# Kernel tuning notes

Measured on AMD Instinct MI355X. Metric: run time of the kernel, lower is better.

## Reference

```python
import jax, jax.numpy as jnp
import numpy as np

# PGA G(3,0,1) blade layout: [1, e0,e1,e2,e3, e01,e02,e03,e12,e13,e23, e012,e013,e023,e123, e0123]
GRADE_IDX = np.array([0,1,1,1,1,2,2,2,2,2,2,3,3,3,3,4])  # grade of each of the 16 blades
INNER_IDX = np.array([0,2,3,4,8,9,10,14])  # non-degenerate blades (no e0) used by invariant inner product
POINT_IDX = np.array([11,12,13])           # trivector point coordinates e012,e013,e023
EPS = 1e-6

def equi_linear(x, W5, b):
    # x: [B,N,Cin,16]; W5: [5,Cout,Cin] grade-wise channel mixing (equivariant)
    Wc = W5[GRADE_IDX]                       # [16,Cout,Cin]
    y = jnp.einsum('bnic,coi->bnoc', x, Wc)  # [B,N,Cout,16]
    return y.at[..., 0].add(b)               # bias only on scalar blade

def equi_rms_norm(x, w):
    # RMS of per-channel multivector norms, averaged over channels
    ms = jnp.mean(jnp.sum(x * x, axis=-1), axis=-1, keepdims=True)  # [B,N,1]
    return x * jax.lax.rsqrt(ms + EPS)[..., None] * w[:, None]

def setup_inputs():
    key = jax.random.key(0)
    ks = jax.random.split(key, 10)
    B, Nq, Nk, C, H = 8, 1024, 256, 48, 8
    s = 0.05
    return {
        'hidden': jax.random.normal(ks[0], (B, Nq, C, 16), jnp.float32),
        'vision_embedding': jax.random.normal(ks[1], (B, Nk, C, 16), jnp.float32),
        'ln_w': jnp.ones((C,), jnp.float32),
        'Wq': jax.random.normal(ks[2], (5, H * C, C), jnp.float32) * s,
        'bq': jnp.zeros((H * C,), jnp.float32),
        'Wkv': jax.random.normal(ks[3], (5, 2 * H * C, C), jnp.float32) * s,
        'bkv': jnp.zeros((2 * H * C,), jnp.float32),
        'Wo': jax.random.normal(ks[4], (5, C, H * C), jnp.float32) * s,
        'bo': jnp.zeros((C,), jnp.float32),
        'daa_scale': jnp.zeros((H,), jnp.float32),
    }

def reference(hidden, vision_embedding, ln_w, Wq, bq, Wkv, bkv, Wo, bo, daa_scale):
    B, Nq, C, _ = hidden.shape
    H = daa_scale.shape[0]
    normed = equi_rms_norm(hidden, ln_w)
    q = equi_linear(normed, Wq, bq).reshape(B, Nq, H, C, 16)
    kv = equi_linear(vision_embedding, Wkv, bkv)
    Nk = kv.shape[1]
    kv = kv.reshape(B, Nk, 2, H, C, 16)
    k, v = kv[:, :, 0], kv[:, :, 1]
    # inner-product attention (ipa) over non-degenerate blades
    qi, ki = q[..., INNER_IDX], k[..., INNER_IDX]
    ipa = jnp.einsum('bqhcj,bkhcj->bhqk', qi, ki) / np.sqrt(8.0 * C)
    # distance-aware attention (daa) on trivector point coords, expanded ||q-k||^2
    qp, kp = q[..., POINT_IDX], k[..., POINT_IDX]
    q2 = jnp.sum(qp * qp, axis=(-1, -2)).transpose(0, 2, 1)  # [B,H,Nq]
    k2 = jnp.sum(kp * kp, axis=(-1, -2)).transpose(0, 2, 1)  # [B,H,Nk]
    cross = jnp.einsum('bqhcj,bkhcj->bhqk', qp, kp)
    dist2 = q2[..., :, None] + k2[..., None, :] - 2.0 * cross
    daa = -jax.nn.softplus(daa_scale)[None, :, None, None] * dist2 / C
    attn = jax.nn.softmax(ipa + daa, axis=-1)                 # [B,H,Nq,Nk]
    out = jnp.einsum('bhqk,bkhcj->bqhcj', attn, v).reshape(B, Nq, H * C, 16)
    return hidden + equi_linear(out, Wo, bo)
```

## Files before the change

### kernel.cpp

```cpp
#include <hip/hip_runtime.h>

typedef unsigned short u16;
typedef unsigned int u32;
typedef unsigned long long u64;

typedef float f32x4 __attribute__((ext_vector_type(4)));
typedef short bf16x8 __attribute__((ext_vector_type(8)));

#define BB 8
#define NQ 1024
#define NK 256
#define HH 8
#define KD 544

__device__ __forceinline__ float bf2f(u16 u) {
  union { u32 i; float f; } v; v.i = ((u32)u) << 16; return v.f;
}
__device__ __forceinline__ u16 f2bf(float f) {
  union { u32 i; float f; } v; v.f = f;
  u32 i = v.i;
  return (u16)((i + 0x7FFFu + ((i >> 16) & 1u)) >> 16);
}
__device__ __forceinline__ float softplusf(float d) {
  return (d > 20.f) ? d : log1pf(__expf(d));
}

#define GRADE_TAB 0x4333322222211110ULL
#define ACT_TAB   0xDCBEA984320ULL
__device__ __forceinline__ int grade_of(int c) { return (int)((GRADE_TAB >> (c * 4)) & 15ULL); }
__device__ __forceinline__ int act_of(int s) { return (int)((ACT_TAB >> (s * 4)) & 15ULL); }

constexpr float INV_S384 = 0.05103103630798288f;

__global__ __launch_bounds__(256) void wB_kernel(
    const float* __restrict__ Wq, const float* __restrict__ Wkv,
    const float* __restrict__ Wo, u16* __restrict__ WqB,
    u16* __restrict__ WkvB, u16* __restrict__ WoB) {
  int idx = blockIdx.x * 256 + threadIdx.x;
  const int NA = 5 * 384 * 64, NB = 5 * 768 * 64, NC = 5 * 48 * 384;
  if (idx < NA) {
    int g = idx / (384 * 64);
    int rem = idx - g * 384 * 64;
    int o = rem >> 6, j = rem & 63;
    WqB[idx] = (j < 48) ? f2bf(Wq[((size_t)g * 384 + o) * 48 + j]) : (u16)0;
  } else if (idx < NA + NB) {
    int k = idx - NA;
    int g = k / (768 * 64);
    int rem = k - g * 768 * 64;
    int o = rem >> 6, j = rem & 63;
    WkvB[k] = (j < 48) ? f2bf(Wkv[((size_t)g * 768 + o) * 48 + j]) : (u16)0;
  } else if (idx < NA + NB + NC) {
    int k = idx - NA - NB;
    WoB[k] = f2bf(Wo[k]);
  }
}

__global__ __launch_bounds__(256) void xJ_kernel(
    const float* __restrict__ src, u16* __restrict__ dst,
    const float* __restrict__ lnw, int NR, int norm) {
  __shared__ __align__(16) float ls[16 * 772];
  __shared__ float rs_s[16];
  const int t = threadIdx.x;
  const int row0 = blockIdx.x * 64;
  const int row16 = t & 15, c = t >> 4;
  for (int chunk = 0; chunk < 4; chunk++) {
    const int r0c = row0 + chunk * 16;
    __syncthreads();
#pragma unroll
    for (int k = 0; k < 12; k++) {
      int f = t + 256 * k;
      int r = f / 192, j = f - r * 192;
      *(float4*)&ls[r * 772 + j * 4] =
          *(const float4*)(src + (size_t)(r0c + r) * 768 + j * 4);
    }
    __syncthreads();
    if (norm) {
      const int r = t >> 4, j16 = t & 15;
      float s = 0.f;
#pragma unroll
      for (int i = 0; i < 12; i++) {
        float4 v = *(const float4*)&ls[r * 772 + j16 * 48 + i * 4];
        s += v.x * v.x + v.y * v.y + v.z * v.z + v.w * v.w;
      }
#pragma unroll
      for (int off = 8; off; off >>= 1) s += __shfl_xor(s, off, 16);
      if (j16 == 0) rs_s[r] = rsqrtf(s * (1.f / 48.f) + 1e-6f);
      __syncthreads();
    }
    const float rsv = norm ? rs_s[row16] : 1.f;
    u16 buf[64];
#pragma unroll
    for (int i = 0; i < 48; i++) {
      float v = ls[row16 * 772 + i * 16 + c];
      if (norm) v *= rsv * lnw[i];
      buf[i] = f2bf(v);
    }
#pragma unroll
    for (int i = 48; i < 64; i++) buf[i] = 0;
    u16* dp = dst + ((size_t)c * NR + r0c + row16) * 64;
#pragma unroll
    for (int j4 = 0; j4 < 8; j4++) *(uint4*)(dp + j4 * 8) = *(uint4*)&buf[j4 * 8];
  }
}

#define QSTR 392
__global__ __launch_bounds__(256) void q_mfma(
    const u16* __restrict__ xq, const u16* __restrict__ WqB,
    const float* __restrict__ bq, const float* __restrict__ daa,
    u16* __restrict__ qsel) {
  __shared__ __align__(16) u16 es[4 * 16 * QSTR];
  const int t = threadIdx.x;
  const int w = t >> 6, lane = t & 63, m16 = lane & 15, quad = lane >> 4;
  const int slot = blockIdx.y;
  const int c = act_of(slot), g = grade_of(c);
  const int row0 = blockIdx.x * 64;
  const int b = row0 >> 10, n0 = row0 & 1023;
  f32x4 acc[24];
#pragma unroll
  for (int nt = 0; nt < 24; nt++) acc[nt] = (f32x4)0.f;
  const u16* ap = xq + ((size_t)c * 8192 + row0 + w * 16 + m16) * 64 + quad * 8;
  const u16* wb = WqB + (size_t)g * 384 * 64 + (size_t)m16 * 64 + quad * 8;
#pragma unroll
  for (int ks = 0; ks < 2; ks++) {
    bf16x8 af = *(const bf16x8*)(ap + ks * 32);
#pragma unroll
    for (int nt = 0; nt < 24; nt++) {
      bf16x8 bf = *(const bf16x8*)(wb + (size_t)nt * 16 * 64 + ks * 32);
      acc[nt] = __builtin_amdgcn_mfma_f32_16x16x32_bf16(af, bf, acc[nt], 0, 0, 0);
    }
  }
#pragma unroll
  for (int nt = 0; nt < 24; nt++) {
    const int o = nt * 16 + m16;
    const int h = o / 48;
    const float sc = (slot < 8) ? INV_S384 : (2.f * softplusf(daa[h]) * (1.f / 48.f));
    const float bias = (slot == 0) ? bq[o] : 0.f;
#pragma unroll
    for (int rr = 0; rr < 4; rr++)
      es[(w * 16 + quad * 4 + rr) * QSTR + o] = f2bf((acc[nt][rr] + bias) * sc);
  }
  __syncthreads();
  for (int ch = t; ch < 512; ch += 256) {
    int r = ch >> 3, h = ch & 7;
    const uint4* sr = (const uint4*)&es[r * QSTR + h * 48];
    u16* dst = qsel + ((size_t)(b * 8 + h) * NQ + n0 + r) * KD + slot * 48;
#pragma unroll
    for (int j = 0; j < 6; j++) ((uint4*)dst)[j] = sr[j];
    if (slot == 10) {
      uint4 z = {0u, 0u, 0u, 0u};
      ((uint4*)dst)[6] = z;
      ((uint4*)dst)[7] = z;
    }
  }
}

#define VSTR 72
__global__ __launch_bounds__(256) void kv_mfma(
    const u16* __restrict__ xv, const u16* __restrict__ WkvB,
    const float* __restrict__ bkv, u16* __restrict__ ksel,
    u16* __restrict__ vT) {
  __shared__ __align__(16) u16 es[384 * VSTR];
  const int t = threadIdx.x;
  const int w = t >> 6, lane = t & 63, m16 = lane & 15, quad = lane >> 4;
  const int task = blockIdx.y;
  const int row0 = blockIdx.x * 64;
  const int b = row0 >> 8, n0 = row0 & 255;

  if (task < 11) {
    const int c = act_of(task), g = grade_of(c);
    f32x4 acc[24];
#pragma unroll
    for (int nt = 0; nt < 24; nt++) acc[nt] = (f32x4)0.f;
    const u16* ap = xv + ((size_t)c * 2048 + row0 + w * 16 + m16) * 64 + quad * 8;
    const u16* wb = WkvB + (size_t)g * 768 * 64 + (size_t)m16 * 64 + quad * 8;
#pragma unroll
    for (int ks = 0; ks < 2; ks++) {
      bf16x8 af = *(const bf16x8*)(ap + ks * 32);
#pragma unroll
      for (int nt = 0; nt < 24; nt++) {
        bf16x8 bf = *(const bf16x8*)(wb + (size_t)nt * 16 * 64 + ks * 32);
        acc[nt] = __builtin_amdgcn_mfma_f32_16x16x32_bf16(af, bf, acc[nt], 0, 0, 0);
      }
    }
#pragma unroll
    for (int nt = 0; nt < 24; nt++) {
      const int o = nt * 16 + m16;
      const float bias = (task == 0) ? bkv[o] : 0.f;
#pragma unroll
      for (int rr = 0; rr < 4; rr++)
        es[(w * 16 + quad * 4 + rr) * QSTR + o] = f2bf(acc[nt][rr] + bias);
    }
    __syncthreads();
    for (int ch = t; ch < 512; ch += 256) {
      int r = ch >> 3, h = ch & 7;
      const uint4* sr = (const uint4*)&es[r * QSTR + h * 48];
      u16* dst = ksel + ((size_t)(b * 8 + h) * NK + n0 + r) * KD + task * 48;
#pragma unroll
      for (int j = 0; j < 6; j++) ((uint4*)dst)[j] = sr[j];
      if (task == 10) {
        uint4 z = {0u, 0u, 0u, 0u};
        ((uint4*)dst)[6] = z;
        ((uint4*)dst)[7] = z;
      }
    }
  } else {
    const int c = task - 11, g = grade_of(c);
    f32x4 acc[24];
#pragma unroll
    for (int nt = 0; nt < 24; nt++) acc[nt] = (f32x4)0.f;
    const u16* ap = xv + ((size_t)c * 2048 + row0 + w * 16 + m16) * 64 + quad * 8;
    const u16* wb = WkvB + (size_t)g * 768 * 64 + (size_t)(384 + m16) * 64 + quad * 8;
#pragma unroll
    for (int ks = 0; ks < 2; ks++) {
      bf16x8 af = *(const bf16x8*)(ap + ks * 32);
#pragma unroll
      for (int nt = 0; nt < 24; nt++) {
        bf16x8 bf = *(const bf16x8*)(wb + (size_t)nt * 16 * 64 + ks * 32);
        acc[nt] = __builtin_amdgcn_mfma_f32_16x16x32_bf16(af, bf, acc[nt], 0, 0, 0);
      }
    }
#pragma unroll
    for (int nt = 0; nt < 24; nt++) {
      const int o = nt * 16 + m16;
      const float bias = (c == 0) ? bkv[384 + o] : 0.f;
#pragma unroll
      for (int rr = 0; rr < 4; rr++)
        es[o * VSTR + w * 16 + quad * 4 + rr] = f2bf(acc[nt][rr] + bias);
    }
    __syncthreads();
    for (int id = t; id < 6144; id += 256) {
      int o = id >> 4, part = id & 15;
      uint2 v = *(const uint2*)&es[o * VSTR + part * 4];
      int h = o / 48, oc = o - h * 48;
      *(uint2*)(vT + ((size_t)(b * 8 + h) * 768 + oc * 16 + c) * 256 + n0 + part * 4) = v;
    }
  }
}

__global__ __launch_bounds__(256) void k2_kernel(const u16* __restrict__ ksel,
                                                 const float* __restrict__ daa,
                                                 float* __restrict__ kbias) {
  int id = blockIdx.x * 256 + threadIdx.x;
  const uint4* p = (const uint4*)(ksel + (size_t)id * KD + 384);
  float s = 0.f;
#pragma unroll
  for (int j = 0; j < 18; j++) {
    uint4 v = p[j];
    u32 a[4] = {v.x, v.y, v.z, v.w};
#pragma unroll
    for (int q = 0; q < 4; q++) {
      float lo = bf2f((u16)(a[q] & 0xFFFFu));
      float hi = bf2f((u16)(a[q] >> 16));
      s += lo * lo + hi * hi;
    }
  }
  int h = (id >> 8) & 7;
  kbias[id] = -(softplusf(daa[h]) * (1.f / 48.f)) * s;
}

#define SPBW 268
#define STGW 26

#define QK_MFMA_BLOCK(AQ0, AQ1, AQ2, AQ3, AK0, AK1, AK2, AK3)                 \
  sacc[0][0] = __builtin_amdgcn_mfma_f32_16x16x32_bf16(AQ0, AK0, sacc[0][0], 0, 0, 0); \
  sacc[1][0] = __builtin_amdgcn_mfma_f32_16x16x32_bf16(AQ1, AK0, sacc[1][0], 0, 0, 0); \
  sacc[2][0] = __builtin_amdgcn_mfma_f32_16x16x32_bf16(AQ2, AK0, sacc[2][0], 0, 0, 0); \
  sacc[3][0] = __builtin_amdgcn_mfma_f32_16x16x32_bf16(AQ3, AK0, sacc[3][0], 0, 0, 0); \
  sacc[0][1] = __builtin_amdgcn_mfma_f32_16x16x32_bf16(AQ0, AK1, sacc[0][1], 0, 0, 0); \
  sacc[1][1] = __builtin_amdgcn_mfma_f32_16x16x32_bf16(AQ1, AK1, sacc[1][1], 0, 0, 0); \
  sacc[2][1] = __builtin_amdgcn_mfma_f32_16x16x32_bf16(AQ2, AK1, sacc[2][1], 0, 0, 0); \
  sacc[3][1] = __builtin_amdgcn_mfma_f32_16x16x32_bf16(AQ3, AK1, sacc[3][1], 0, 0, 0); \
  sacc[0][2] = __builtin_amdgcn_mfma_f32_16x16x32_bf16(AQ0, AK2, sacc[0][2], 0, 0, 0); \
  sacc[1][2] = __builtin_amdgcn_mfma_f32_16x16x32_bf16(AQ1, AK2, sacc[1][2], 0, 0, 0); \
  sacc[2][2] = __builtin_amdgcn_mfma_f32_16x16x32_bf16(AQ2, AK2, sacc[2][2], 0, 0, 0); \
  sacc[3][2] = __builtin_amdgcn_mfma_f32_16x16x32_bf16(AQ3, AK2, sacc[3][2], 0, 0, 0); \
  sacc[0][3] = __builtin_amdgcn_mfma_f32_16x16x32_bf16(AQ0, AK3, sacc[0][3], 0, 0, 0); \
  sacc[1][3] = __builtin_amdgcn_mfma_f32_16x16x32_bf16(AQ1, AK3, sacc[1][3], 0, 0, 0); \
  sacc[2][3] = __builtin_amdgcn_mfma_f32_16x16x32_bf16(AQ2, AK3, sacc[2][3], 0, 0, 0); \
  sacc[3][3] = __builtin_amdgcn_mfma_f32_16x16x32_bf16(AQ3, AK3, sacc[3][3], 0, 0, 0);

__global__ __launch_bounds__(256, 2) void attn_kernel(
    const u16* __restrict__ qsel, const u16* __restrict__ ksel,
    const float* __restrict__ kbias, const u16* __restrict__ vT,
    u16* __restrict__ ctxJ) {
  const int qt = blockIdx.x, h = blockIdx.y, b = blockIdx.z;
  const int g = b * 8 + h;

  const int t = threadIdx.x;
  const int w = t >> 6;
  const int lane = t & 63;
  const int m16 = lane & 15;
  const int quad = lane >> 4;

  __shared__ __align__(16) u32 uni_s[13312];
  u16* spb = (u16*)uni_s;
  u32* stg = uni_s;
  __shared__ float kb[256];
  __shared__ __align__(16) float wred[64][4];
  __shared__ __align__(16) float wsum[64][4];

  const size_t bh = (size_t)g;
  const int n0 = qt * 64;
  const u16* qg = qsel + (bh * NQ + n0) * KD;
  const u16* kg = ksel + bh * NK * KD;
  const u16* vg = vT + bh * 768 * 256;

  kb[t] = kbias[bh * NK + t];
  __syncthreads();
  float kbr[4];
#pragma unroll
  for (int nt = 0; nt < 4; nt++) kbr[nt] = kb[w * 64 + nt * 16 + m16];

  f32x4 sacc[4][4];
#pragma unroll
  for (int mt = 0; mt < 4; mt++)
#pragma unroll
    for (int nt = 0; nt < 4; nt++) sacc[mt][nt] = (f32x4)0.f;

  const u16* qp0 = qg + (size_t)m16 * KD + quad * 8;
  const u16* qp1 = qg + (size_t)(16 + m16) * KD + quad * 8;
  const u16* qp2 = qg + (size_t)(32 + m16) * KD + quad * 8;
  const u16* qp3 = qg + (size_t)(48 + m16) * KD + quad * 8;
  const u16* kp = kg + (size_t)(w * 64 + m16) * KD + quad * 8;
  bf16x8 cq0 = *(const bf16x8*)qp0;
  bf16x8 cq1 = *(const bf16x8*)qp1;
  bf16x8 cq2 = *(const bf16x8*)qp2;
  bf16x8 cq3 = *(const bf16x8*)qp3;
  bf16x8 ck0 = *(const bf16x8*)(kp);
  bf16x8 ck1 = *(const bf16x8*)(kp + 16 * KD);
  bf16x8 ck2 = *(const bf16x8*)(kp + 32 * KD);
  bf16x8 ck3 = *(const bf16x8*)(kp + 48 * KD);
  bf16x8 dq0 = *(const bf16x8*)(qp0 + 32);
  bf16x8 dq1 = *(const bf16x8*)(qp1 + 32);
  bf16x8 dq2 = *(const bf16x8*)(qp2 + 32);
  bf16x8 dq3 = *(const bf16x8*)(qp3 + 32);
  bf16x8 dk0 = *(const bf16x8*)(kp + 32);
  bf16x8 dk1 = *(const bf16x8*)(kp + 16 * KD + 32);
  bf16x8 dk2 = *(const bf16x8*)(kp + 32 * KD + 32);
  bf16x8 dk3 = *(const bf16x8*)(kp + 48 * KD + 32);
  for (int i = 0; i < 7; i++) {
    const int oA = (2 * i + 2) * 32;
    bf16x8 nq0 = *(const bf16x8*)(qp0 + oA);
    bf16x8 nq1 = *(const bf16x8*)(qp1 + oA);
    bf16x8 nq2 = *(const bf16x8*)(qp2 + oA);
    bf16x8 nq3 = *(const bf16x8*)(qp3 + oA);
    bf16x8 nk0 = *(const bf16x8*)(kp + oA);
    bf16x8 nk1 = *(const bf16x8*)(kp + 16 * KD + oA);
    bf16x8 nk2 = *(const bf16x8*)(kp + 32 * KD + oA);
    bf16x8 nk3 = *(const bf16x8*)(kp + 48 * KD + oA);
    const int oB = (2 * i + 3) * 32;
    bf16x8 mq0 = *(const bf16x8*)(qp0 + oB);
    bf16x8 mq1 = *(const bf16x8*)(qp1 + oB);
    bf16x8 mq2 = *(const bf16x8*)(qp2 + oB);
    bf16x8 mq3 = *(const bf16x8*)(qp3 + oB);
    bf16x8 mk0 = *(const bf16x8*)(kp + oB);
    bf16x8 mk1 = *(const bf16x8*)(kp + 16 * KD + oB);
    bf16x8 mk2 = *(const bf16x8*)(kp + 32 * KD + oB);
    bf16x8 mk3 = *(const bf16x8*)(kp + 48 * KD + oB);
    QK_MFMA_BLOCK(cq0, cq1, cq2, cq3, ck0, ck1, ck2, ck3)
    QK_MFMA_BLOCK(dq0, dq1, dq2, dq3, dk0, dk1, dk2, dk3)
    cq0 = nq0; cq1 = nq1; cq2 = nq2; cq3 = nq3;
    ck0 = nk0; ck1 = nk1; ck2 = nk2; ck3 = nk3;
    dq0 = mq0; dq1 = mq1; dq2 = mq2; dq3 = mq3;
    dk0 = mk0; dk1 = mk1; dk2 = mk2; dk3 = mk3;
  }
  {
    const int oT = 16 * 32;
    bf16x8 nq0 = *(const bf16x8*)(qp0 + oT);
    bf16x8 nq1 = *(const bf16x8*)(qp1 + oT);
    bf16x8 nq2 = *(const bf16x8*)(qp2 + oT);
    bf16x8 nq3 = *(const bf16x8*)(qp3 + oT);
    bf16x8 nk0 = *(const bf16x8*)(kp + oT);
    bf16x8 nk1 = *(const bf16x8*)(kp + 16 * KD + oT);
    bf16x8 nk2 = *(const bf16x8*)(kp + 32 * KD + oT);
    bf16x8 nk3 = *(const bf16x8*)(kp + 48 * KD + oT);
    QK_MFMA_BLOCK(cq0, cq1, cq2, cq3, ck0, ck1, ck2, ck3)
    QK_MFMA_BLOCK(dq0, dq1, dq2, dq3, dk0, dk1, dk2, dk3)
    QK_MFMA_BLOCK(nq0, nq1, nq2, nq3, nk0, nk1, nk2, nk3)
  }

#pragma unroll
  for (int mt = 0; mt < 4; mt++)
#pragma unroll
    for (int rr = 0; rr < 4; rr++) {
      float a0 = sacc[mt][0][rr] + kbr[0];
      float a1 = sacc[mt][1][rr] + kbr[1];
      float a2 = sacc[mt][2][rr] + kbr[2];
      float a3 = sacc[mt][3][rr] + kbr[3];
      sacc[mt][0][rr] = a0; sacc[mt][1][rr] = a1;
      sacc[mt][2][rr] = a2; sacc[mt][3][rr] = a3;
      float m = fmaxf(fmaxf(a0, a1), fmaxf(a2, a3));
#pragma unroll
      for (int off = 1; off < 16; off <<= 1)
        m = fmaxf(m, __shfl_xor(m, off));
      if (m16 == mt * 4 + rr) wred[mt * 16 + quad * 4 + rr][w] = m;
    }
  __syncthreads();
#pragma unroll
  for (int mt = 0; mt < 4; mt++)
#pragma unroll
    for (int rr = 0; rr < 4; rr++) {
      const int row = mt * 16 + quad * 4 + rr;
      float4 m4 = *(const float4*)wred[row];
      const float gm = fmaxf(fmaxf(m4.x, m4.y), fmaxf(m4.z, m4.w));
      float s = 0.f;
#pragma unroll
      for (int nt = 0; nt < 4; nt++) {
        float e = __expf(sacc[mt][nt][rr] - gm);
        s += e;
        spb[row * SPBW + w * 64 + nt * 16 + m16] = f2bf(e);
      }
#pragma unroll
      for (int off = 1; off < 16; off <<= 1)
        s += __shfl_xor(s, off);
      if (m16 == mt * 4 + rr) wsum[row][w] = s;
    }
  __syncthreads();

  f32x4 oacc[4][12];
#pragma unroll
  for (int mt = 0; mt < 4; mt++)
#pragma unroll
    for (int nt = 0; nt < 12; nt++) oacc[mt][nt] = (f32x4)0.f;

  const u16* vp = vg + (size_t)(w * 192 + m16) * 256 + quad * 8;
  bf16x8 vc[12];
#pragma unroll
  for (int nt = 0; nt < 12; nt++)
    vc[nt] = *(const bf16x8*)(vp + (size_t)nt * 16 * 256);
#pragma unroll
  for (int ks = 0; ks < 8; ks++) {
    bf16x8 vn[12];
    if (ks < 7) {
#pragma unroll
      for (int nt = 0; nt < 12; nt++)
        vn[nt] = *(const bf16x8*)(vp + (size_t)nt * 16 * 256 + (ks + 1) * 32);
    }
    bf16x8 pa0 = *(const bf16x8*)(&spb[(size_t)m16 * SPBW + ks * 32 + quad * 8]);
    bf16x8 pa1 = *(const bf16x8*)(&spb[(size_t)(16 + m16) * SPBW + ks * 32 + quad * 8]);
    bf16x8 pa2 = *(const bf16x8*)(&spb[(size_t)(32 + m16) * SPBW + ks * 32 + quad * 8]);
    bf16x8 pa3 = *(const bf16x8*)(&spb[(size_t)(48 + m16) * SPBW + ks * 32 + quad * 8]);
#pragma unroll
    for (int nt = 0; nt < 12; nt++) {
      oacc[0][nt] = __builtin_amdgcn_mfma_f32_16x16x32_bf16(pa0, vc[nt], oacc[0][nt], 0, 0, 0);
      oacc[1][nt] = __builtin_amdgcn_mfma_f32_16x16x32_bf16(pa1, vc[nt], oacc[1][nt], 0, 0, 0);
      oacc[2][nt] = __builtin_amdgcn_mfma_f32_16x16x32_bf16(pa2, vc[nt], oacc[2][nt], 0, 0, 0);
      oacc[3][nt] = __builtin_amdgcn_mfma_f32_16x16x32_bf16(pa3, vc[nt], oacc[3][nt], 0, 0, 0);
    }
    if (ks < 7) {
#pragma unroll
      for (int nt = 0; nt < 12; nt++) vc[nt] = vn[nt];
    }
  }

  const size_t rowbase = (size_t)b * NQ + n0;
#pragma unroll
  for (int ch2 = 0; ch2 < 2; ch2++) {
    __syncthreads();
    if ((m16 >> 3) == ch2) {
      const int c8 = m16 & 7;
#pragma unroll
      for (int mt = 0; mt < 4; mt++)
#pragma unroll
        for (int rr = 0; rr < 4; rr++) {
          const int row = mt * 16 + quad * 4 + rr;
          float4 s4 = *(const float4*)wsum[row];
          const float iv = 1.f / (s4.x + s4.y + s4.z + s4.w);
          u32* dp = stg + (row * 8 + c8) * STGW + w * 6;
#pragma unroll
          for (int j = 0; j < 6; j++) {
            u32 lo = f2bf(oacc[mt][2 * j][rr] * iv);
            u32 hi = f2bf(oacc[mt][2 * j + 1][rr] * iv);
            dp[j] = lo | (hi << 16);
          }
        }
    }
    __syncthreads();
    for (int ch = t; ch < 512; ch += 256) {
      const int prow = ch >> 3, pc8 = ch & 7;
      const u32* sp2 = stg + (prow * 8 + pc8) * STGW;
      u16* dst = ctxJ + ((size_t)(ch2 * 8 + pc8) * 8192 + rowbase + prow) * 384 + h * 48;
#pragma unroll
      for (int j6 = 0; j6 < 6; j6++) {
        uint2 a = *(const uint2*)(sp2 + j6 * 4);
        uint2 bb2 = *(const uint2*)(sp2 + j6 * 4 + 2);
        uint4 v4v = {a.x, a.y, bb2.x, bb2.y};
        *(uint4*)(dst + j6 * 8) = v4v;
      }
    }
  }
}

#define ESTR2 785
__global__ __launch_bounds__(1024) void out_kernel(
    const u16* __restrict__ ctxJ, const u16* __restrict__ WoB,
    const float* __restrict__ bo, const float* __restrict__ hidden,
    float* __restrict__ out) {
  __shared__ __align__(16) float es[16 * ESTR2];
  const int t = threadIdx.x;
  const int c = __builtin_amdgcn_readfirstlane(t >> 6);
  const int lane = t & 63;
  const int m16 = lane & 15, quad = lane >> 4;
  const int r0 = blockIdx.x * 16;
  const int g = grade_of(c);
  const u16* wb = WoB + (size_t)g * 48 * 384;

  f32x4 acc[3];
#pragma unroll
  for (int nt = 0; nt < 3; nt++) acc[nt] = (f32x4)0.f;
  const u16* ap = ctxJ + ((size_t)c * 8192 + r0 + m16) * 384 + quad * 8;
#pragma unroll 4
  for (int ks = 0; ks < 12; ks++) {
    bf16x8 af = *(const bf16x8*)(ap + ks * 32);
#pragma unroll
    for (int nt = 0; nt < 3; nt++) {
      bf16x8 bf = *(const bf16x8*)(wb + (size_t)(nt * 16 + m16) * 384 + ks * 32 + quad * 8);
      acc[nt] = __builtin_amdgcn_mfma_f32_16x16x32_bf16(af, bf, acc[nt], 0, 0, 0);
    }
  }
  __syncthreads();
#pragma unroll
  for (int nt = 0; nt < 3; nt++)
#pragma unroll
    for (int rr = 0; rr < 4; rr++)
      es[(quad * 4 + rr) * ESTR2 + c * 49 + nt * 16 + m16] = acc[nt][rr];
  __syncthreads();
#pragma unroll
  for (int k = 0; k < 3; k++) {
    int m4 = t + 1024 * k;
    int r = m4 / 192;
    int col0 = (m4 - r * 192) * 4;
    int o = col0 >> 4, cb = col0 & 15;
    const float* er = &es[r * ESTR2 + o];
    float4 v;
    v.x = er[(cb + 0) * 49];
    v.y = er[(cb + 1) * 49];
    v.z = er[(cb + 2) * 49];
    v.w = er[(cb + 3) * 49];
    if (cb == 0) v.x += bo[o];
    size_t gidx = (size_t)(r0 + r) * 768 + col0;
    const float4 hv = *(const float4*)&hidden[gidx];
    v.x += hv.x; v.y += hv.y; v.z += hv.z; v.w += hv.w;
    *(float4*)&out[gidx] = v;
  }
}

extern "C" void kernel_launch(void* const* d_in, const int* in_sizes, int n_in,
                              void* d_out, int out_size, void* d_ws, size_t ws_size,
                              hipStream_t stream) {
  const float* hidden = (const float*)d_in[0];
  const float* vis = (const float*)d_in[1];
  const float* lnw = (const float*)d_in[2];
  const float* Wq = (const float*)d_in[3];
  const float* bq = (const float*)d_in[4];
  const float* Wkv = (const float*)d_in[5];
  const float* bkv = (const float*)d_in[6];
  const float* Wo = (const float*)d_in[7];
  const float* bo = (const float*)d_in[8];
  const float* daa = (const float*)d_in[9];
  float* out = (float*)d_out;

  char* ws = (char*)d_ws;
  size_t off = 0;
  auto carve = [&](size_t bytes) -> void* {
    void* p = ws + off;
    off += (bytes + 255) & ~(size_t)255;
    return p;
  };
  u16* WqB = (u16*)carve((size_t)5 * 384 * 64 * 2);
  u16* WkvB = (u16*)carve((size_t)5 * 768 * 64 * 2);
  u16* WoB = (u16*)carve((size_t)5 * 48 * 384 * 2);
  u16* qsel = (u16*)carve((size_t)BB * HH * NQ * KD * 2);
  u16* ksel = (u16*)carve((size_t)BB * HH * NK * KD * 2);
  u16* vT = (u16*)carve((size_t)BB * HH * 768 * 256 * 2);
  float* kbias = (float*)carve((size_t)BB * HH * NK * 4);
  char* uni = (char*)carve((size_t)16 * 384 * 8192 * 2);
  u16* ctxJ = (u16*)uni;
  u16* xq = (u16*)uni;
  u16* xv = (u16*)(uni + (size_t)16 * 8192 * 64 * 2);

  wB_kernel<<<1800, 256, 0, stream>>>(Wq, Wkv, Wo, WqB, WkvB, WoB);
  xJ_kernel<<<BB * NQ / 64, 256, 0, stream>>>(hidden, xq, lnw, BB * NQ, 1);
  xJ_kernel<<<BB * NK / 64, 256, 0, stream>>>(vis, xv, nullptr, BB * NK, 0);
  kv_mfma<<<dim3(BB * NK / 64, 27), 256, 0, stream>>>(xv, WkvB, bkv, ksel, vT);
  k2_kernel<<<64, 256, 0, stream>>>(ksel, daa, kbias);
  q_mfma<<<dim3(BB * NQ / 64, 11), 256, 0, stream>>>(xq, WqB, bq, daa, qsel);
  attn_kernel<<<dim3(NQ / 64, HH, BB), 256, 0, stream>>>(qsel, ksel, kbias, vT, ctxJ);
  out_kernel<<<512, 1024, 0, stream>>>(ctxJ, WoB, bo, hidden, out);
}
```

Baseline: 443.5 us.

## Merge projection kernels and fold key-norm computation into KV projection

```diff
diff --git a/kernel.cpp b/kernel.cpp
--- a/kernel.cpp
+++ b/kernel.cpp
@@ -35,9 +35,11 @@
 __global__ __launch_bounds__(256) void wB_kernel(
     const float* __restrict__ Wq, const float* __restrict__ Wkv,
     const float* __restrict__ Wo, u16* __restrict__ WqB,
-    u16* __restrict__ WkvB, u16* __restrict__ WoB) {
+    u16* __restrict__ WkvB, u16* __restrict__ WoB,
+    float* __restrict__ kbias) {
   int idx = blockIdx.x * 256 + threadIdx.x;
   const int NA = 5 * 384 * 64, NB = 5 * 768 * 64, NC = 5 * 48 * 384;
+  if (idx < BB * HH * NK) kbias[idx] = 0.f;
   if (idx < NA) {
     int g = idx / (384 * 64);
     int rem = idx - g * 384 * 64;
@@ -56,12 +58,18 @@
 }
 
 __global__ __launch_bounds__(256) void xJ_kernel(
-    const float* __restrict__ src, u16* __restrict__ dst,
-    const float* __restrict__ lnw, int NR, int norm) {
+    const float* __restrict__ hidden, const float* __restrict__ vis,
+    u16* __restrict__ xq, u16* __restrict__ xv,
+    const float* __restrict__ lnw) {
   __shared__ __align__(16) float ls[16 * 772];
   __shared__ float rs_s[16];
   const int t = threadIdx.x;
-  const int row0 = blockIdx.x * 64;
+  const int bid = blockIdx.x;
+  const float* src;
+  u16* dst;
+  int NR, norm, row0;
+  if (bid < 128) { src = hidden; dst = xq; NR = 8192; norm = 1; row0 = bid * 64; }
+  else           { src = vis;    dst = xv; NR = 2048; norm = 0; row0 = (bid - 128) * 64; }
   const int row16 = t & 15, c = t >> 4;
   for (int chunk = 0; chunk < 4; chunk++) {
     const int r0c = row0 + chunk * 16;
@@ -104,66 +112,67 @@
 }
 
 #define QSTR 392
-__global__ __launch_bounds__(256) void q_mfma(
-    const u16* __restrict__ xq, const u16* __restrict__ WqB,
-    const float* __restrict__ bq, const float* __restrict__ daa,
-    u16* __restrict__ qsel) {
-  __shared__ __align__(16) u16 es[4 * 16 * QSTR];
-  const int t = threadIdx.x;
-  const int w = t >> 6, lane = t & 63, m16 = lane & 15, quad = lane >> 4;
-  const int slot = blockIdx.y;
-  const int c = act_of(slot), g = grade_of(c);
-  const int row0 = blockIdx.x * 64;
-  const int b = row0 >> 10, n0 = row0 & 1023;
-  f32x4 acc[24];
-#pragma unroll
-  for (int nt = 0; nt < 24; nt++) acc[nt] = (f32x4)0.f;
-  const u16* ap = xq + ((size_t)c * 8192 + row0 + w * 16 + m16) * 64 + quad * 8;
-  const u16* wb = WqB + (size_t)g * 384 * 64 + (size_t)m16 * 64 + quad * 8;
-#pragma unroll
-  for (int ks = 0; ks < 2; ks++) {
-    bf16x8 af = *(const bf16x8*)(ap + ks * 32);
-#pragma unroll
-    for (int nt = 0; nt < 24; nt++) {
-      bf16x8 bf = *(const bf16x8*)(wb + (size_t)nt * 16 * 64 + ks * 32);
-      acc[nt] = __builtin_amdgcn_mfma_f32_16x16x32_bf16(af, bf, acc[nt], 0, 0, 0);
-    }
-  }
-#pragma unroll
-  for (int nt = 0; nt < 24; nt++) {
-    const int o = nt * 16 + m16;
-    const int h = o / 48;
-    const float sc = (slot < 8) ? INV_S384 : (2.f * softplusf(daa[h]) * (1.f / 48.f));
-    const float bias = (slot == 0) ? bq[o] : 0.f;
-#pragma unroll
-    for (int rr = 0; rr < 4; rr++)
-      es[(w * 16 + quad * 4 + rr) * QSTR + o] = f2bf((acc[nt][rr] + bias) * sc);
-  }
-  __syncthreads();
-  for (int ch = t; ch < 512; ch += 256) {
-    int r = ch >> 3, h = ch & 7;
-    const uint4* sr = (const uint4*)&es[r * QSTR + h * 48];
-    u16* dst = qsel + ((size_t)(b * 8 + h) * NQ + n0 + r) * KD + slot * 48;
-#pragma unroll
-    for (int j = 0; j < 6; j++) ((uint4*)dst)[j] = sr[j];
-    if (slot == 10) {
-      uint4 z = {0u, 0u, 0u, 0u};
-      ((uint4*)dst)[6] = z;
-      ((uint4*)dst)[7] = z;
-    }
-  }
-}
-
 #define VSTR 72
-__global__ __launch_bounds__(256) void kv_mfma(
-    const u16* __restrict__ xv, const u16* __restrict__ WkvB,
-    const float* __restrict__ bkv, u16* __restrict__ ksel,
-    u16* __restrict__ vT) {
+__global__ __launch_bounds__(256) void qkv_mfma(
+    const u16* __restrict__ xq, const u16* __restrict__ xv,
+    const u16* __restrict__ WqB, const u16* __restrict__ WkvB,
+    const float* __restrict__ bq, const float* __restrict__ bkv,
+    const float* __restrict__ daa, u16* __restrict__ qsel,
+    u16* __restrict__ ksel, u16* __restrict__ vT,
+    float* __restrict__ kbias) {
   __shared__ __align__(16) u16 es[384 * VSTR];
   const int t = threadIdx.x;
   const int w = t >> 6, lane = t & 63, m16 = lane & 15, quad = lane >> 4;
-  const int task = blockIdx.y;
-  const int row0 = blockIdx.x * 64;
+  const int bid = blockIdx.x;
+
+  if (bid < 1408) {
+    const int rowblk = bid & 127, slot = bid >> 7;
+    const int c = act_of(slot), g = grade_of(c);
+    const int row0 = rowblk * 64;
+    const int b = row0 >> 10, n0 = row0 & 1023;
+    f32x4 acc[24];
+#pragma unroll
+    for (int nt = 0; nt < 24; nt++) acc[nt] = (f32x4)0.f;
+    const u16* ap = xq + ((size_t)c * 8192 + row0 + w * 16 + m16) * 64 + quad * 8;
+    const u16* wb = WqB + (size_t)g * 384 * 64 + (size_t)m16 * 64 + quad * 8;
+#pragma unroll
+    for (int ks = 0; ks < 2; ks++) {
+      bf16x8 af = *(const bf16x8*)(ap + ks * 32);
+#pragma unroll
+      for (int nt = 0; nt < 24; nt++) {
+        bf16x8 bf = *(const bf16x8*)(wb + (size_t)nt * 16 * 64 + ks * 32);
+        acc[nt] = __builtin_amdgcn_mfma_f32_16x16x32_bf16(af, bf, acc[nt], 0, 0, 0);
+      }
+    }
+#pragma unroll
+    for (int nt = 0; nt < 24; nt++) {
+      const int o = nt * 16 + m16;
+      const int h = o / 48;
+      const float sc = (slot < 8) ? INV_S384 : (2.f * softplusf(daa[h]) * (1.f / 48.f));
+      const float bias = (slot == 0) ? bq[o] : 0.f;
+#pragma unroll
+      for (int rr = 0; rr < 4; rr++)
+        es[(w * 16 + quad * 4 + rr) * QSTR + o] = f2bf((acc[nt][rr] + bias) * sc);
+    }
+    __syncthreads();
+    for (int ch = t; ch < 512; ch += 256) {
+      int r = ch >> 3, h = ch & 7;
+      const uint4* sr = (const uint4*)&es[r * QSTR + h * 48];
+      u16* dst = qsel + ((size_t)(b * 8 + h) * NQ + n0 + r) * KD + slot * 48;
+#pragma unroll
+      for (int j = 0; j < 6; j++) ((uint4*)dst)[j] = sr[j];
+      if (slot == 10) {
+        uint4 z = {0u, 0u, 0u, 0u};
+        ((uint4*)dst)[6] = z;
+        ((uint4*)dst)[7] = z;
+      }
+    }
+    return;
+  }
+
+  const int kvid = bid - 1408;
+  const int keyblk = kvid & 31, task = kvid >> 5;
+  const int row0 = keyblk * 64;
   const int b = row0 >> 8, n0 = row0 & 255;
 
   if (task < 11) {
@@ -203,6 +212,16 @@
         ((uint4*)dst)[7] = z;
       }
     }
+    if (task >= 8) {
+      for (int id = t; id < 512; id += 256) {
+        int r = id >> 3, hh = id & 7;
+        const u16* er = &es[r * QSTR + hh * 48];
+        float s = 0.f;
+#pragma unroll
+        for (int oc = 0; oc < 48; oc++) { float v = bf2f(er[oc]); s += v * v; }
+        atomicAdd(&kbias[((size_t)(b * 8 + hh)) * NK + n0 + r], s);
+      }
+    }
   } else {
     const int c = task - 11, g = grade_of(c);
     f32x4 acc[24];
@@ -235,27 +254,6 @@
       *(uint2*)(vT + ((size_t)(b * 8 + h) * 768 + oc * 16 + c) * 256 + n0 + part * 4) = v;
     }
   }
-}
-
-__global__ __launch_bounds__(256) void k2_kernel(const u16* __restrict__ ksel,
-                                                 const float* __restrict__ daa,
-                                                 float* __restrict__ kbias) {
-  int id = blockIdx.x * 256 + threadIdx.x;
-  const uint4* p = (const uint4*)(ksel + (size_t)id * KD + 384);
-  float s = 0.f;
-#pragma unroll
-  for (int j = 0; j < 18; j++) {
-    uint4 v = p[j];
-    u32 a[4] = {v.x, v.y, v.z, v.w};
-#pragma unroll
-    for (int q = 0; q < 4; q++) {
-      float lo = bf2f((u16)(a[q] & 0xFFFFu));
-      float hi = bf2f((u16)(a[q] >> 16));
-      s += lo * lo + hi * hi;
-    }
-  }
-  int h = (id >> 8) & 7;
-  kbias[id] = -(softplusf(daa[h]) * (1.f / 48.f)) * s;
 }
 
 #define SPBW 268
@@ -281,8 +279,8 @@
 
 __global__ __launch_bounds__(256, 2) void attn_kernel(
     const u16* __restrict__ qsel, const u16* __restrict__ ksel,
-    const float* __restrict__ kbias, const u16* __restrict__ vT,
-    u16* __restrict__ ctxJ) {
+    const float* __restrict__ kbias, const float* __restrict__ daa,
+    const u16* __restrict__ vT, u16* __restrict__ ctxJ) {
   const int qt = blockIdx.x, h = blockIdx.y, b = blockIdx.z;
   const int g = b * 8 + h;
 
@@ -305,7 +303,8 @@
   const u16* kg = ksel + bh * NK * KD;
   const u16* vg = vT + bh * 768 * 256;
 
-  kb[t] = kbias[bh * NK + t];
+  const float ksc = -(softplusf(daa[h]) * (1.f / 48.f));
+  kb[t] = ksc * kbias[bh * NK + t];
   __syncthreads();
   float kbr[4];
 #pragma unroll
@@ -579,12 +578,11 @@
   u16* xq = (u16*)uni;
   u16* xv = (u16*)(uni + (size_t)16 * 8192 * 64 * 2);
 
-  wB_kernel<<<1800, 256, 0, stream>>>(Wq, Wkv, Wo, WqB, WkvB, WoB);
-  xJ_kernel<<<BB * NQ / 64, 256, 0, stream>>>(hidden, xq, lnw, BB * NQ, 1);
-  xJ_kernel<<<BB * NK / 64, 256, 0, stream>>>(vis, xv, nullptr, BB * NK, 0);
-  kv_mfma<<<dim3(BB * NK / 64, 27), 256, 0, stream>>>(xv, WkvB, bkv, ksel, vT);
-  k2_kernel<<<64, 256, 0, stream>>>(ksel, daa, kbias);
-  q_mfma<<<dim3(BB * NQ / 64, 11), 256, 0, stream>>>(xq, WqB, bq, daa, qsel);
-  attn_kernel<<<dim3(NQ / 64, HH, BB), 256, 0, stream>>>(qsel, ksel, kbias, vT, ctxJ);
+  wB_kernel<<<1800, 256, 0, stream>>>(Wq, Wkv, Wo, WqB, WkvB, WoB, kbias);
+  xJ_kernel<<<160, 256, 0, stream>>>(hidden, vis, xq, xv, lnw);
+  qkv_mfma<<<2272, 256, 0, stream>>>(xq, xv, WqB, WkvB, bq, bkv, daa,
+                                     qsel, ksel, vT, kbias);
+  attn_kernel<<<dim3(NQ / 64, HH, BB), 256, 0, stream>>>(qsel, ksel, kbias,
+                                                          daa, vT, ctxJ);
   out_kernel<<<512, 1024, 0, stream>>>(ctxJ, WoB, bo, hidden, out);
 }
```

Result: no change. 445.5 us (+0.4%).
